# Kernel tuning notes

Hardware: AMD Instinct MI355X
Metric: run time of the kernel (lower is better)

Reference implementation:

```python
import jax, jax.numpy as jnp
import numpy as np

N = 50000        # num_nodes
E = 800000       # num_edges (avg degree 16)
F_IN = 128
F_OUT = 128
ALPHA = 0.2      # LeakyReLU negative slope
EPS = 1e-12


def setup_inputs() -> dict:
    key = jax.random.key(0)
    k1, k2, k3, k4 = jax.random.split(key, 4)
    input_ = jax.random.normal(k1, (N, F_IN), jnp.float32)
    # xavier_normal-like scale to keep exp() well-behaved
    W = jax.random.normal(k2, (F_OUT, 2 * F_IN), jnp.float32) * (1.414 * (2.0 / (F_OUT + 2 * F_IN)) ** 0.5)
    a = jax.random.normal(k3, (1, F_OUT), jnp.float32) * (1.414 * (2.0 / (1 + F_OUT)) ** 0.5)
    edge = jax.random.randint(k4, (2, E), 0, N, jnp.int32)
    return {"input_": input_, "W": W, "a": a, "edge": edge}


def reference(input_, W, a, edge):
    src = edge[0]  # row index used by the sparse scatter (sum over dim=1 -> grouped by edge[0])
    dst = edge[1]
    # gather endpoint features and concat: [E, 2*F_in]
    edge_h = jnp.concatenate([input_[src], input_[dst]], axis=1)
    # per-edge linear transform: [E, F_out]  (torch: W.mm(edge_h^T) -> transposed layout)
    edge_m = edge_h @ W.T
    # per-edge attention logit and unnormalized coefficient: [E]
    scores = edge_m @ a[0]
    edge_e = jnp.exp(-jax.nn.leaky_relu(scores, ALPHA))
    # denominator: segment-sum of edge_e over source nodes, [N]
    e_row_sum = jax.ops.segment_sum(edge_e, src, num_segments=N)
    e_row_sum = jnp.where(e_row_sum == 0.0, EPS, e_row_sum)
    # numerator: segment-sum of weighted messages, [N, F_out]
    h_prime = jax.ops.segment_sum(edge_e[:, None] * edge_m, src, num_segments=N)
    h_prime = h_prime / e_row_sum[:, None]
    return jax.nn.elu(h_prime)  # concat=True path
```

## Files before the change

### kernel.cpp

```cpp
#include <hip/hip_runtime.h>

#define NN 50000
#define NE 800000
#define ALPHA 0.2f
#define BCAP 64

typedef unsigned int u32;
typedef unsigned short u16t;

using frag  = __attribute__((ext_vector_type(8))) short;
using f32x4 = __attribute__((ext_vector_type(4))) float;

__device__ __forceinline__ float bf2f(u16t v) { return __uint_as_float(((u32)v) << 16); }
__device__ __forceinline__ u16t f2bf(float f) {
    u32 x = __float_as_uint(f);
    u32 r = x + 0x7fffu + ((x >> 16) & 1u);
    return (u16t)(r >> 16);
}

__global__ void k_wb(const float* __restrict__ W, u16t* __restrict__ WbSeq,
                     int* __restrict__ cnt) {
    int o = blockIdx.x * 256 + threadIdx.x;
    if (o < 32768) {
        int j = o & 7, fid = o >> 3;
        int quad = fid & 3, col = (fid >> 2) & 15, ks = (fid >> 6) & 3, nt = fid >> 8;
        int fp = nt * 16 + col;
        int k = ks * 32 + quad * 8 + j;
        float v = (fp < 128) ? W[fp * 256 + k] : W[(fp - 128) * 256 + 128 + k];
        WbSeq[o] = f2bf(v);
    }
    if (o < NN) cnt[o] = 0;
}

__global__ __launch_bounds__(256) void k_gemm(
        const float* __restrict__ X, const u16t* __restrict__ WbSeq,
        const float* __restrict__ A,
        float* __restrict__ Hs, u16t* __restrict__ Hd,
        float* __restrict__ s1, float* __restrict__ s2) {
    const int tid  = threadIdx.x;
    const int wave = tid >> 6;
    const int lane = tid & 63;
    const int mt   = blockIdx.x * 4 + wave;
    if (mt >= 3125) return;
    const int col  = lane & 15;
    const int quad = lane >> 4;
    const int node0 = mt * 16;
    const int laneoff = col * 4 + quad;

    frag afrag[4];
    const float* xrow = X + (size_t)(node0 + col) * 128;
#pragma unroll
    for (int ks = 0; ks < 4; ++ks) {
        const float4* p = (const float4*)(xrow + ks * 32 + quad * 8);
        float4 v0 = p[0], v1 = p[1];
        frag a;
        a[0] = (short)f2bf(v0.x); a[1] = (short)f2bf(v0.y);
        a[2] = (short)f2bf(v0.z); a[3] = (short)f2bf(v0.w);
        a[4] = (short)f2bf(v1.x); a[5] = (short)f2bf(v1.y);
        a[6] = (short)f2bf(v1.z); a[7] = (short)f2bf(v1.w);
        afrag[ks] = a;
    }

    f32x4 acc[16];
#pragma unroll
    for (int nt = 0; nt < 16; ++nt)
#pragma unroll
        for (int r = 0; r < 4; ++r) acc[nt][r] = 0.f;

    const frag* WbF = (const frag*)WbSeq;
#pragma unroll
    for (int nt = 0; nt < 16; ++nt) {
#pragma unroll
        for (int ks = 0; ks < 4; ++ks) {
            frag b = WbF[nt * 256 + ks * 64 + laneoff];
            acc[nt] = __builtin_amdgcn_mfma_f32_16x16x32_bf16(afrag[ks], b, acc[nt], 0, 0, 0);
        }
    }

#pragma unroll
    for (int r = 0; r < 4; ++r) {
        float p1 = 0.f, p2 = 0.f;
#pragma unroll
        for (int nt = 0; nt < 8; ++nt)  p1 += acc[nt][r] * A[nt * 16 + col];
#pragma unroll
        for (int nt = 8; nt < 16; ++nt) p2 += acc[nt][r] * A[(nt - 8) * 16 + col];
        p1 += __shfl_xor(p1, 1); p1 += __shfl_xor(p1, 2);
        p1 += __shfl_xor(p1, 4); p1 += __shfl_xor(p1, 8);
        p2 += __shfl_xor(p2, 1); p2 += __shfl_xor(p2, 2);
        p2 += __shfl_xor(p2, 4); p2 += __shfl_xor(p2, 8);
        if (col == 0) {
            int node = node0 + quad * 4 + r;
            s1[node] = p1;
            s2[node] = p2;
        }
    }

#pragma unroll
    for (int nt = 0; nt < 8; ++nt)
#pragma unroll
        for (int r = 0; r < 4; ++r)
            Hs[(size_t)(node0 + quad * 4 + r) * 128 + nt * 16 + col] = acc[nt][r];
#pragma unroll
    for (int nt = 8; nt < 16; ++nt)
#pragma unroll
        for (int r = 0; r < 4; ++r)
            Hd[(size_t)(node0 + quad * 4 + r) * 128 + (nt - 8) * 16 + col] = f2bf(acc[nt][r]);
}

__global__ void k_bucket(const int* __restrict__ srcArr,
                         const int* __restrict__ dstArr,
                         int* __restrict__ cnt, u16t* __restrict__ bucket) {
    int e = blockIdx.x * 256 + threadIdx.x;
    if (e < NE) {
        int s = srcArr[e];
        int d = dstArr[e];
        if (s < 0 || s >= NN) return;
        int slot = atomicAdd(&cnt[s], 1);
        if (slot < BCAP)
            bucket[(size_t)s * BCAP + slot] = (u16t)d;
    }
}

__global__ __launch_bounds__(256) void k_agg(
        const int* __restrict__ cnt, const u16t* __restrict__ bucket,
        const float* __restrict__ s1, const float* __restrict__ s2,
        const float* __restrict__ Hs, const u16t* __restrict__ Hd,
        float* __restrict__ out) {
    __shared__ float wls[4][BCAP];
    __shared__ int   dls[4][BCAP];
    const int wave = threadIdx.x >> 6;
    const int lane = threadIdx.x & 63;
    const int i = blockIdx.x * 4 + wave;

    int deg = cnt[i];
    deg = (deg < 0) ? 0 : ((deg > BCAP) ? BCAP : deg);
    float w = 0.f; int dl = 0;
    if (lane < deg) {
        dl = (int)bucket[(size_t)i * BCAP + lane];
        if (dl >= NN) dl = 0;
        float sc = s1[i] + s2[dl];
        sc = fminf(fmaxf(sc, -80.f), 80.f);
        w = __expf(-fmaxf(sc, ALPHA * sc));
    }
    wls[wave][lane] = w;
    dls[wave][lane] = dl;
    float S = w;
    S += __shfl_xor(S, 1);  S += __shfl_xor(S, 2);  S += __shfl_xor(S, 4);
    S += __shfl_xor(S, 8);  S += __shfl_xor(S, 16); S += __shfl_xor(S, 32);
    __syncthreads();

    const int g  = lane >> 4;
    const int fb = (lane & 15) * 8;
    float acc[8];
#pragma unroll
    for (int k = 0; k < 8; ++k) acc[k] = 0.f;

    const int iters = (deg + 3) >> 2;
    int j = 0;
    for (; j + 1 < iters; j += 2) {
        int e0 = j * 4 + g, e1 = e0 + 4;
        float w0 = wls[wave][e0], w1 = wls[wave][e1];
        int   d0 = dls[wave][e0], d1 = dls[wave][e1];
        uint4 h0 = *(const uint4*)&Hd[(size_t)d0 * 128 + fb];
        uint4 h1 = *(const uint4*)&Hd[(size_t)d1 * 128 + fb];
        acc[0] += w0 * bf2f((u16t)(h0.x & 0xffff)); acc[1] += w0 * bf2f((u16t)(h0.x >> 16));
        acc[2] += w0 * bf2f((u16t)(h0.y & 0xffff)); acc[3] += w0 * bf2f((u16t)(h0.y >> 16));
        acc[4] += w0 * bf2f((u16t)(h0.z & 0xffff)); acc[5] += w0 * bf2f((u16t)(h0.z >> 16));
        acc[6] += w0 * bf2f((u16t)(h0.w & 0xffff)); acc[7] += w0 * bf2f((u16t)(h0.w >> 16));
        acc[0] += w1 * bf2f((u16t)(h1.x & 0xffff)); acc[1] += w1 * bf2f((u16t)(h1.x >> 16));
        acc[2] += w1 * bf2f((u16t)(h1.y & 0xffff)); acc[3] += w1 * bf2f((u16t)(h1.y >> 16));
        acc[4] += w1 * bf2f((u16t)(h1.z & 0xffff)); acc[5] += w1 * bf2f((u16t)(h1.z >> 16));
        acc[6] += w1 * bf2f((u16t)(h1.w & 0xffff)); acc[7] += w1 * bf2f((u16t)(h1.w >> 16));
    }
    if (j < iters) {
        int e0 = j * 4 + g;
        float w0 = wls[wave][e0];
        int   d0 = dls[wave][e0];
        uint4 h0 = *(const uint4*)&Hd[(size_t)d0 * 128 + fb];
        acc[0] += w0 * bf2f((u16t)(h0.x & 0xffff)); acc[1] += w0 * bf2f((u16t)(h0.x >> 16));
        acc[2] += w0 * bf2f((u16t)(h0.y & 0xffff)); acc[3] += w0 * bf2f((u16t)(h0.y >> 16));
        acc[4] += w0 * bf2f((u16t)(h0.z & 0xffff)); acc[5] += w0 * bf2f((u16t)(h0.z >> 16));
        acc[6] += w0 * bf2f((u16t)(h0.w & 0xffff)); acc[7] += w0 * bf2f((u16t)(h0.w >> 16));
    }

#pragma unroll
    for (int k = 0; k < 8; ++k) {
        acc[k] += __shfl_xor(acc[k], 16);
        acc[k] += __shfl_xor(acc[k], 32);
    }

    if (lane < 16) {
        float4 o0 = make_float4(0.f, 0.f, 0.f, 0.f), o1 = o0;
        if (deg > 0) {
            float inv = 1.f / fmaxf(S, 1e-12f);
            const float* hsrow = Hs + (size_t)i * 128 + fb;
            float4 hs0 = *(const float4*)hsrow;
            float4 hs1 = *(const float4*)(hsrow + 4);
            float h;
            h = hs0.x + acc[0] * inv; o0.x = (h > 0.f) ? h : (__expf(h) - 1.f);
            h = hs0.y + acc[1] * inv; o0.y = (h > 0.f) ? h : (__expf(h) - 1.f);
            h = hs0.z + acc[2] * inv; o0.z = (h > 0.f) ? h : (__expf(h) - 1.f);
            h = hs0.w + acc[3] * inv; o0.w = (h > 0.f) ? h : (__expf(h) - 1.f);
            h = hs1.x + acc[4] * inv; o1.x = (h > 0.f) ? h : (__expf(h) - 1.f);
            h = hs1.y + acc[5] * inv; o1.y = (h > 0.f) ? h : (__expf(h) - 1.f);
            h = hs1.z + acc[6] * inv; o1.z = (h > 0.f) ? h : (__expf(h) - 1.f);
            h = hs1.w + acc[7] * inv; o1.w = (h > 0.f) ? h : (__expf(h) - 1.f);
        }
        float* orow = out + (size_t)i * 128 + fb;
        *(float4*)orow = o0;
        *(float4*)(orow + 4) = o1;
    }
}

extern "C" void kernel_launch(void* const* d_in, const int* in_sizes, int n_in,
                              void* d_out, int out_size, void* d_ws, size_t ws_size,
                              hipStream_t stream) {
    const float* X = (const float*)d_in[0];
    const float* W = (const float*)d_in[1];
    const float* A = (const float*)d_in[2];
    const int* edge = (const int*)d_in[3];
    const int* srcArr = edge;
    const int* dstArr = edge + NE;
    float* out = (float*)d_out;

    char* ws = (char*)d_ws;
    size_t off = 0;
    auto alloc = [&](size_t bytes) {
        void* p = ws + off;
        off = (off + bytes + 255) & ~(size_t)255;
        return p;
    };
    float* Hs  = (float*)alloc((size_t)NN * 128 * 4);
    u16t*  Hd  = (u16t*)alloc((size_t)NN * 128 * 2);
    float* s1  = (float*)alloc((size_t)NN * 4);
    float* s2  = (float*)alloc((size_t)NN * 4);
    int*   cnt = (int*)alloc((size_t)NN * 4);
    u16t*  bkt = (u16t*)alloc((size_t)NN * BCAP * 2);
    u16t*  Wb  = (u16t*)alloc(256 * 128 * 2);
    (void)ws_size; (void)in_sizes; (void)n_in; (void)out_size;

    k_wb<<<196, 256, 0, stream>>>(W, Wb, cnt);
    k_bucket<<<NE / 256, 256, 0, stream>>>(srcArr, dstArr, cnt, bkt);
    k_gemm<<<782, 256, 0, stream>>>(X, Wb, A, Hs, Hd, s1, s2);
    k_agg<<<NN / 4, 256, 0, stream>>>(cnt, bkt, s1, s2, Hs, Hd, out);
}
```

Before: 188.1 us.

## Replace per-node global atomic bucketing with two-level binned counting sort

The single bucketing kernel, which did one global atomic per edge on 50k per-node counters, becomes two passes. The first pass packs each (src,dst) pair into one word and appends it to one of 196 coarse bins of 256 source nodes using global atomics. The second pass has one block per bin that fills the per-node buckets using shared-memory atomics, so the scattered 2-byte writes land in a compact region and counts are written without a separate zeroing step. In exchange it adds a kernel launch, an intermediate array, and heavy atomic contention on only 196 global counters.

```diff
diff --git a/kernel.cpp b/kernel.cpp
--- a/kernel.cpp
+++ b/kernel.cpp
@@ -4,6 +4,8 @@
 #define NE 800000
 #define ALPHA 0.2f
 #define BCAP 64
+#define NB 196
+#define BINCAP 5120
 
 typedef unsigned int u32;
 typedef unsigned short u16t;
@@ -19,17 +21,57 @@
 }
 
 __global__ void k_wb(const float* __restrict__ W, u16t* __restrict__ WbSeq,
-                     int* __restrict__ cnt) {
+                     int* __restrict__ binCnt) {
     int o = blockIdx.x * 256 + threadIdx.x;
-    if (o < 32768) {
-        int j = o & 7, fid = o >> 3;
-        int quad = fid & 3, col = (fid >> 2) & 15, ks = (fid >> 6) & 3, nt = fid >> 8;
-        int fp = nt * 16 + col;
-        int k = ks * 32 + quad * 8 + j;
-        float v = (fp < 128) ? W[fp * 256 + k] : W[(fp - 128) * 256 + 128 + k];
-        WbSeq[o] = f2bf(v);
-    }
-    if (o < NN) cnt[o] = 0;
+    int j = o & 7, fid = o >> 3;
+    int quad = fid & 3, col = (fid >> 2) & 15, ks = (fid >> 6) & 3, nt = fid >> 8;
+    int fp = nt * 16 + col;
+    int k = ks * 32 + quad * 8 + j;
+    float v = (fp < 128) ? W[fp * 256 + k] : W[(fp - 128) * 256 + 128 + k];
+    WbSeq[o] = f2bf(v);
+    if (o < NB * 16) binCnt[o] = 0;
+}
+
+__global__ void k_place(const int* __restrict__ srcArr,
+                        const int* __restrict__ dstArr,
+                        int* __restrict__ binCnt, u32* __restrict__ sorted) {
+    int e = blockIdx.x * 256 + threadIdx.x;
+    if (e < NE) {
+        int s = srcArr[e];
+        int d = dstArr[e];
+        if (s < 0 || s >= NN) return;
+        int b = s >> 8;
+        int pos = atomicAdd(&binCnt[b * 16], 1);
+        if (pos < BINCAP)
+            sorted[(size_t)b * BINCAP + pos] = ((u32)s << 16) | (u32)d;
+    }
+}
+
+__global__ __launch_bounds__(256) void k_fill(
+        const int* __restrict__ binCnt, const u32* __restrict__ sorted,
+        int* __restrict__ cnt, u16t* __restrict__ bucket) {
+    __shared__ int lcnt[256];
+    const int b = blockIdx.x;
+    const int tid = threadIdx.x;
+    lcnt[tid] = 0;
+    __syncthreads();
+    int count = binCnt[b * 16];
+    if (count > BINCAP) count = BINCAP;
+    const u32* mybin = sorted + (size_t)b * BINCAP;
+    for (int base = 0; base < count; base += 256) {
+        int e = base + tid;
+        if (e < count) {
+            u32 key = mybin[e];
+            int sl = (key >> 16) & 255;
+            int d  = key & 0xffff;
+            int slot = atomicAdd(&lcnt[sl], 1);
+            if (slot < BCAP)
+                bucket[((size_t)(b * 256 + sl)) * BCAP + slot] = (u16t)d;
+        }
+    }
+    __syncthreads();
+    int s = b * 256 + tid;
+    if (s < NN) cnt[s] = lcnt[tid];
 }
 
 __global__ __launch_bounds__(256) void k_gemm(
@@ -105,20 +147,6 @@
 #pragma unroll
         for (int r = 0; r < 4; ++r)
             Hd[(size_t)(node0 + quad * 4 + r) * 128 + (nt - 8) * 16 + col] = f2bf(acc[nt][r]);
-}
-
-__global__ void k_bucket(const int* __restrict__ srcArr,
-                         const int* __restrict__ dstArr,
-                         int* __restrict__ cnt, u16t* __restrict__ bucket) {
-    int e = blockIdx.x * 256 + threadIdx.x;
-    if (e < NE) {
-        int s = srcArr[e];
-        int d = dstArr[e];
-        if (s < 0 || s >= NN) return;
-        int slot = atomicAdd(&cnt[s], 1);
-        if (slot < BCAP)
-            bucket[(size_t)s * BCAP + slot] = (u16t)d;
-    }
 }
 
 __global__ __launch_bounds__(256) void k_agg(
@@ -230,17 +258,20 @@
         off = (off + bytes + 255) & ~(size_t)255;
         return p;
     };
-    float* Hs  = (float*)alloc((size_t)NN * 128 * 4);
-    u16t*  Hd  = (u16t*)alloc((size_t)NN * 128 * 2);
-    float* s1  = (float*)alloc((size_t)NN * 4);
-    float* s2  = (float*)alloc((size_t)NN * 4);
-    int*   cnt = (int*)alloc((size_t)NN * 4);
-    u16t*  bkt = (u16t*)alloc((size_t)NN * BCAP * 2);
-    u16t*  Wb  = (u16t*)alloc(256 * 128 * 2);
+    float* Hs   = (float*)alloc((size_t)NN * 128 * 4);
+    u16t*  Hd   = (u16t*)alloc((size_t)NN * 128 * 2);
+    float* s1   = (float*)alloc((size_t)NN * 4);
+    float* s2   = (float*)alloc((size_t)NN * 4);
+    int*   cnt  = (int*)alloc((size_t)NN * 4);
+    u16t*  bkt  = (u16t*)alloc((size_t)NN * BCAP * 2);
+    u16t*  Wb   = (u16t*)alloc(256 * 128 * 2);
+    int*   binC = (int*)alloc((size_t)NB * 16 * 4);
+    u32*   sorted = (u32*)alloc((size_t)NB * BINCAP * 4);
     (void)ws_size; (void)in_sizes; (void)n_in; (void)out_size;
 
-    k_wb<<<196, 256, 0, stream>>>(W, Wb, cnt);
-    k_bucket<<<NE / 256, 256, 0, stream>>>(srcArr, dstArr, cnt, bkt);
+    k_wb<<<128, 256, 0, stream>>>(W, Wb, binC);
+    k_place<<<(NE + 255) / 256, 256, 0, stream>>>(srcArr, dstArr, binC, sorted);
+    k_fill<<<NB, 256, 0, stream>>>(binC, sorted, cnt, bkt);
     k_gemm<<<782, 256, 0, stream>>>(X, Wb, A, Hs, Hd, s1, s2);
     k_agg<<<NN / 4, 256, 0, stream>>>(cnt, bkt, s1, s2, Hs, Hd, out);
 }
```

New measurement: 233.2 us. 24.0% more time.
